# Kernel tuning notes

Measured on AMD Instinct MI355X. Metric: run time of the kernel, lower is better.

The kernel has to match this reference:

```python
import jax, jax.numpy as jnp
import numpy as np

EPS = 0.0  # torch.norm has no eps; faithful division by exact L2 norms


def reference(x1, x2):
    # x1: [B, h_w, C] query local descriptors
    # x2: [n_domain, n_way, n_shot, h_w, C]; discriminator=False -> use domain 0
    B, h_w, C = x1.shape
    _, n_way, n_shot, _, _ = x2.shape
    support = x2[0].reshape(n_way * n_shot, h_w, C)  # [S, h_w, C]

    # Original math: Sim[i,b,j,c] = <q_ij, s_bc> / (||q_ij|| * ||s_bc||), then sum over j,c.
    # Because the norm denominator factorizes, the double spatial sum collapses:
    #   sum_{j,c} (q_ij/||q_ij||) . (s_bc/||s_bc||) = (sum_j q_ij/||q_ij||) . (sum_c s_bc/||s_bc||)
    # Same values, without materializing the [B, S, h_w, h_w] tensor.
    q_norm = jnp.linalg.norm(x1, axis=2, keepdims=True)          # [B, h_w, 1]
    s_norm = jnp.linalg.norm(support, axis=2, keepdims=True)      # [S, h_w, 1]
    q_bar = (x1 / q_norm).sum(axis=1)                             # [B, C]
    s_bar = (support / s_norm).sum(axis=1)                        # [S, C]
    return jnp.einsum('ic,bc->ib', q_bar, s_bar)                  # [B, n_way*n_shot]


def setup_inputs() -> dict:
    key = jax.random.key(0)
    k1, k2 = jax.random.split(key)
    x1 = jax.random.normal(k1, (75, 441, 64), dtype=jnp.float32)
    x2 = jax.random.normal(k2, (1, 5, 5, 441, 64), dtype=jnp.float32)
    return {"x1": x1, "x2": x2}
```

## Files before the change

### kernel.cpp

```cpp
#include <hip/hip_runtime.h>


#define N_QUERY   75
#define N_SUPPORT 25
#define N_IMG     (N_QUERY + N_SUPPORT)
#define HW        441
#define C         64
#define NCHUNK    21
#define ROWS      21

__global__ __launch_bounds__(128) void bar_accum_kernel(
    const float* __restrict__ x1,
    const float* __restrict__ x2,
    float* __restrict__ bar ) {

    const int chunk = blockIdx.x;
    const int img   = blockIdx.y;
    const int tid   = threadIdx.x;
    const int lane  = tid & 63;
    const int wave  = tid >> 6;

    const float* src = (img < N_QUERY)
        ? (x1 + (size_t)img * HW * C)
        : (x2 + (size_t)(img - N_QUERY) * HW * C);
    const float* base = src + (size_t)chunk * ROWS * C;

    __shared__ float ssp[ROWS][4];
    __shared__ float rnorm[ROWS];

    if (tid < ROWS * 4) {
        const int row = tid >> 2;
        const int seg = tid & 3;
        const float4* p = (const float4*)(base + row * C + seg * 16);
        float ss = 0.f;
        #pragma unroll
        for (int k = 0; k < 4; ++k) {
            float4 v = p[k];
            ss += v.x * v.x + v.y * v.y + v.z * v.z + v.w * v.w;
        }
        ssp[row][seg] = ss;
    }
    __syncthreads();
    if (tid < ROWS)
        rnorm[tid] = rsqrtf(ssp[tid][0] + ssp[tid][1] + ssp[tid][2] + ssp[tid][3]);
    __syncthreads();

    float acc = 0.f;
    #pragma unroll
    for (int jj = wave; jj < ROWS; jj += 2)
        acc += base[jj * C + lane] * rnorm[jj];

    atomicAdd(&bar[img * C + lane], acc);
}

__global__ __launch_bounds__(256) void dot_kernel(
    const float* __restrict__ bar,
    float* __restrict__ out ) {

    const int i    = blockIdx.x;
    const int lane = threadIdx.x & 63;
    const int wave = threadIdx.x >> 6;

    const float q = bar[i * C + lane];
    for (int b = wave; b < N_SUPPORT; b += 4) {
        float p = q * bar[(N_QUERY + b) * C + lane];
        #pragma unroll
        for (int m = 1; m < 64; m <<= 1)
            p += __shfl_xor(p, m, 64);
        if (lane == 0) out[i * N_SUPPORT + b] = p;
    }
}

extern "C" void kernel_launch(void* const* d_in, const int* in_sizes, int n_in,
                              void* d_out, int out_size, void* d_ws, size_t ws_size,
                              hipStream_t stream) {
    const float* x1 = (const float*)d_in[0];
    const float* x2 = (const float*)d_in[1];
    float* out = (float*)d_out;
    float* bar = (float*)d_ws;

    hipMemsetAsync(bar, 0, (size_t)N_IMG * C * sizeof(float), stream);

    dim3 grid1(NCHUNK, N_IMG);
    bar_accum_kernel<<<grid1, 128, 0, stream>>>(x1, x2, bar);
    dot_kernel<<<N_QUERY, 256, 0, stream>>>(bar, out);
}
```

Measured before the change: 70.95 us.

## Fuse bar accumulation and dot product into one kernel via last-block counters

Merges the two kernels into one launch. Each block writes its per-chunk partial sum to a workspace slot instead of using float atomics. A per-image arrival counter lets the last chunk block reduce the partials into the image's bar vector, and a global counter lets the very last block compute all 75x25 dot products. This removes one kernel launch and makes the reduction order deterministic, but the final dot products are serialized onto a single 128-thread block and extra threadfences are added.

```diff
diff --git a/kernel.cpp b/kernel.cpp
--- a/kernel.cpp
+++ b/kernel.cpp
@@ -9,10 +9,13 @@
 #define NCHUNK    21
 #define ROWS      21
 
-__global__ __launch_bounds__(128) void bar_accum_kernel(
+__global__ __launch_bounds__(128) void fused_kernel(
     const float* __restrict__ x1,
     const float* __restrict__ x2,
-    float* __restrict__ bar ) {
+    float* __restrict__ barp ,
+    float* __restrict__ bar  ,
+    unsigned* __restrict__ cnt ,
+    float* __restrict__ out  ) {
 
     const int chunk = blockIdx.x;
     const int img   = blockIdx.y;
@@ -27,6 +30,8 @@
 
     __shared__ float ssp[ROWS][4];
     __shared__ float rnorm[ROWS];
+    __shared__ float red[2][C];
+    __shared__ unsigned s_old;
 
     if (tid < ROWS * 4) {
         const int row = tid >> 2;
@@ -49,25 +54,45 @@
     #pragma unroll
     for (int jj = wave; jj < ROWS; jj += 2)
         acc += base[jj * C + lane] * rnorm[jj];
+    red[wave][lane] = acc;
+    __syncthreads();
+    if (wave == 0)
+        barp[((size_t)img * NCHUNK + chunk) * C + lane] =
+            red[0][lane] + red[1][lane];
 
-    atomicAdd(&bar[img * C + lane], acc);
-}
+    __threadfence();
+    __syncthreads();
+    if (tid == 0) s_old = atomicAdd(&cnt[img], 1u);
+    __syncthreads();
+    if (s_old != NCHUNK - 1) return;
 
-__global__ __launch_bounds__(256) void dot_kernel(
-    const float* __restrict__ bar,
-    float* __restrict__ out ) {
+    __threadfence();
+    if (tid < C) {
+        float s = 0.f;
+        #pragma unroll
+        for (int k = 0; k < NCHUNK; ++k)
+            s += barp[((size_t)img * NCHUNK + k) * C + tid];
+        bar[img * C + tid] = s;
+    }
+    __threadfence();
+    __syncthreads();
+    if (tid == 0) s_old = atomicAdd(&cnt[N_IMG], 1u);
+    __syncthreads();
+    if (s_old != N_IMG - 1) return;
 
-    const int i    = blockIdx.x;
-    const int lane = threadIdx.x & 63;
-    const int wave = threadIdx.x >> 6;
-
-    const float q = bar[i * C + lane];
-    for (int b = wave; b < N_SUPPORT; b += 4) {
-        float p = q * bar[(N_QUERY + b) * C + lane];
+    __threadfence();
+    for (int f = tid; f < N_QUERY * N_SUPPORT; f += 128) {
+        const int i = f / N_SUPPORT;
+        const int b = f - i * N_SUPPORT;
+        const float4* q = (const float4*)(bar + i * C);
+        const float4* s = (const float4*)(bar + (N_QUERY + b) * C);
+        float a = 0.f;
         #pragma unroll
-        for (int m = 1; m < 64; m <<= 1)
-            p += __shfl_xor(p, m, 64);
-        if (lane == 0) out[i * N_SUPPORT + b] = p;
+        for (int k = 0; k < 16; ++k) {
+            float4 u = q[k], v = s[k];
+            a += u.x * v.x + u.y * v.y + u.z * v.z + u.w * v.w;
+        }
+        out[f] = a;
     }
 }
 
@@ -77,11 +102,13 @@
     const float* x1 = (const float*)d_in[0];
     const float* x2 = (const float*)d_in[1];
     float* out = (float*)d_out;
-    float* bar = (float*)d_ws;
 
-    hipMemsetAsync(bar, 0, (size_t)N_IMG * C * sizeof(float), stream);
+    float*    barp = (float*)d_ws;
+    float*    bar  = barp + (size_t)N_IMG * NCHUNK * C;
+    unsigned* cnt  = (unsigned*)(bar + (size_t)N_IMG * C);
 
-    dim3 grid1(NCHUNK, N_IMG);
-    bar_accum_kernel<<<grid1, 128, 0, stream>>>(x1, x2, bar);
-    dot_kernel<<<N_QUERY, 256, 0, stream>>>(bar, out);
+    hipMemsetAsync(cnt, 0, (N_IMG + 1) * sizeof(unsigned), stream);
+
+    dim3 grid(NCHUNK, N_IMG);
+    fused_kernel<<<grid, 128, 0, stream>>>(x1, x2, barp, bar, cnt, out);
 }
```

New measurement: 163.5 us. 2.3x slower.
